# Kernel tuning notes

Hardware: AMD Instinct MI355X
Metric: run time of the kernel (lower is better)

Reference implementation:

```python
import jax, jax.numpy as jnp
import numpy as np
from jax import lax

B, L, D, H = 2, 2048, 2048, 16
DH = D // H            # 128 head dim
D_REL = 64             # relevance projection dim (class const)
K = max(1, int(0.25 * L))  # top-K_FRAC tokens per query
NEG_INF = float('-inf')


def setup_inputs() -> dict:
    key = jax.random.key(0)
    ks = jax.random.split(key, 8)
    s = D ** (-0.5)
    return {
        'hidden_states': jax.random.normal(ks[0], (B, L, D), jnp.float32),
        'relevance':     jax.random.normal(ks[1], (B, L, D), jnp.float32),
        # torch nn.Linear weights are [out_features, in_features]
        'W_q_rel': jax.random.normal(ks[2], (D_REL, D), jnp.float32) * s,
        'W_k_rel': jax.random.normal(ks[3], (D_REL, D), jnp.float32) * s,
        'W_q': jax.random.normal(ks[4], (D, D), jnp.float32) * s,
        'W_k': jax.random.normal(ks[5], (D, D), jnp.float32) * s,
        'W_v': jax.random.normal(ks[6], (D, D), jnp.float32) * s,
        'W_o': jax.random.normal(ks[7], (D, D), jnp.float32) * s,
    }


def _rel_scores(relevance, W_q_rel, W_k_rel):
    # low-rank relevance logits, causally masked: [B, L, L]
    q = relevance @ W_q_rel.T   # [B, L, d_rel]
    k = relevance @ W_k_rel.T   # [B, L, d_rel]
    scores = jnp.einsum('bqd,bkd->bqk', q, k) * (D_REL ** -0.5)
    future = jnp.triu(jnp.ones((L, L), dtype=bool), k=1)
    return jnp.where(future[None], NEG_INF, scores)


def _sparse_mask(rel_scores):
    # additive mask [B, 1, L, L]: top-k per query row -> 0.0, else -inf; diag 0.0
    _, topk_idx = lax.top_k(rel_scores, K)            # [B, L, K]
    b = jnp.arange(B)[:, None, None]
    q = jnp.arange(L)[None, :, None]
    mask = jnp.full((B, L, L), NEG_INF, dtype=rel_scores.dtype)
    mask = mask.at[b, q, topk_idx].set(0.0)
    diag = jnp.arange(L)
    mask = mask.at[:, diag, diag].set(0.0)
    return mask[:, None]  # [B, 1, L, L]


def _attention(hidden_states, W_q, W_k, W_v, W_o, add_mask):
    # standard multi-head attention with additive mask (the wrapped frozen attn)
    q = (hidden_states @ W_q.T).reshape(B, L, H, DH)
    k = (hidden_states @ W_k.T).reshape(B, L, H, DH)
    v = (hidden_states @ W_v.T).reshape(B, L, H, DH)
    scores = jnp.einsum('bqhd,bkhd->bhqk', q, k) * (DH ** -0.5)
    scores = scores + add_mask                      # [B, H, L, L]
    p = jax.nn.softmax(scores, axis=-1)
    ctx = jnp.einsum('bhqk,bkhd->bqhd', p, v).reshape(B, L, D)
    return ctx @ W_o.T


def reference(hidden_states, relevance, W_q_rel, W_k_rel, W_q, W_k, W_v, W_o):
    # Phase 1 path (step >= SPARSE_FROM), no external attention_mask:
    # combined = causal(-inf upper-tri) + sparse top-k mask.
    rel = _rel_scores(relevance, W_q_rel, W_k_rel)
    sparse = _sparse_mask(rel)                      # [B, 1, L, L]
    future = jnp.triu(jnp.ones((L, L), dtype=bool), k=1)
    causal = jnp.where(future, NEG_INF, 0.0).astype(hidden_states.dtype)
    combined = causal[None, None] + sparse          # [B, 1, L, L]
    return _attention(hidden_states, W_q, W_k, W_v, W_o, combined)
```

## Files before the change

### kernel.cpp

```cpp
#include <hip/hip_runtime.h>
#include <math.h>
#include <stdint.h>

#define Bb 2
#define Lq 2048
#define Dm 2048
#define Hh 16
#define DH 128
#define DREL 64
#define KTOP 512

#define NEG_INF (-__builtin_huge_valf())

typedef __attribute__((ext_vector_type(8))) short bf16x8;
typedef __attribute__((ext_vector_type(4))) float f32x4;

static __device__ __forceinline__ unsigned short f2bf(float f) {
  unsigned int u = __float_as_uint(f);
  u += 0x7fffu + ((u >> 16) & 1u);
  return (unsigned short)(u >> 16);
}

static __device__ __forceinline__ void gload16(const void* g, void* lds) {
  __builtin_amdgcn_global_load_lds(
      (const __attribute__((address_space(1))) uint32_t*)(uintptr_t)g,
      (__attribute__((address_space(3))) uint32_t*)(uint32_t)(uintptr_t)lds,
      16, 0, 0);
}

__global__ __launch_bounds__(256) void conv_bf16(const float* __restrict__ in,
                                                 unsigned short* __restrict__ out,
                                                 int n8, float scale) {
  const int i = blockIdx.x * 256 + threadIdx.x;
  if (i >= n8) return;
  const float4 f0 = ((const float4*)in)[2 * i];
  const float4 f1 = ((const float4*)in)[2 * i + 1];
  bf16x8 o;
  o[0] = (short)f2bf(f0.x * scale); o[1] = (short)f2bf(f0.y * scale);
  o[2] = (short)f2bf(f0.z * scale); o[3] = (short)f2bf(f0.w * scale);
  o[4] = (short)f2bf(f1.x * scale); o[5] = (short)f2bf(f1.y * scale);
  o[6] = (short)f2bf(f1.z * scale); o[7] = (short)f2bf(f1.w * scale);
  *(bf16x8*)(out + 8 * (size_t)i) = o;
}

__global__ __launch_bounds__(256) void conv_bf16_w4(const float* __restrict__ w0,
                                                    const float* __restrict__ w1,
                                                    const float* __restrict__ w2,
                                                    const float* __restrict__ w3,
                                                    unsigned short* __restrict__ out,
                                                    float s0) {
  const int sel = blockIdx.y;
  const float* in = (sel == 0) ? w0 : (sel == 1) ? w1 : (sel == 2) ? w2 : w3;
  const float scale = (sel == 0) ? s0 : 1.0f;
  const int i = blockIdx.x * 256 + threadIdx.x;
  const float4 f0 = ((const float4*)in)[2 * i];
  const float4 f1 = ((const float4*)in)[2 * i + 1];
  bf16x8 o;
  o[0] = (short)f2bf(f0.x * scale); o[1] = (short)f2bf(f0.y * scale);
  o[2] = (short)f2bf(f0.z * scale); o[3] = (short)f2bf(f0.w * scale);
  o[4] = (short)f2bf(f1.x * scale); o[5] = (short)f2bf(f1.y * scale);
  o[6] = (short)f2bf(f1.z * scale); o[7] = (short)f2bf(f1.w * scale);
  *(bf16x8*)(out + (size_t)sel * Dm * Dm + 8 * (size_t)i) = o;
}

template <int MF, bool BF16OUT>
__global__ __launch_bounds__(512, 4) void gemmP(const unsigned short* __restrict__ A,
                                                const unsigned short* __restrict__ W,
                                                void* __restrict__ Cv,
                                                int M, int N, int Kd) {
  constexpr int BM = MF * 32;
  __shared__ unsigned short As[2][BM][32];
  __shared__ unsigned short Bs[2][256][32];

  const int tid = threadIdx.x;
  const int lane = tid & 63;
  const int w = tid >> 6;
  const int l15 = lane & 15;
  const int quad = lane >> 4;
  const int wm = w >> 2;
  const int wn = w & 3;

  const int gy = M / BM;
  const int nwg = gy * (N >> 8);
  const int cpx = nwg >> 3;
  const int bid = (int)blockIdx.x;
  const int lin = (bid & 7) * cpx + (bid >> 3);
  const int by = lin % gy, bx = lin / gy;
  const int m0 = by * BM, n0 = bx * 256;

  const int srow = tid >> 2;
  const int sslot = (tid & 3) ^ ((tid >> 3) & 3);
  const unsigned short* aB = A + (size_t)(m0 + srow) * Kd + sslot * 8;
  const unsigned short* bB = W + (size_t)(n0 + srow) * Kd + sslot * 8;
  const size_t hstep = (size_t)128 * Kd;

  f32x4 acc[MF][4];
#pragma unroll
  for (int i = 0; i < MF; ++i)
#pragma unroll
    for (int j = 0; j < 4; ++j) acc[i][j] = (f32x4){0.f, 0.f, 0.f, 0.f};

  bf16x8 af[MF], bfr[2];
  const int rswz = (quad ^ ((l15 >> 1) & 3)) * 8;

#define ST(BUF, T)                                                          \
  do {                                                                      \
    const size_t ko = (size_t)(T) * 32;                                     \
    gload16(aB + ko, &As[BUF][w * 16][0]);                                  \
    if constexpr (MF == 8) gload16(aB + hstep + ko, &As[BUF][(MF == 8 ? 128 : 0) + w * 16][0]); \
    gload16(bB + ko, &Bs[BUF][w * 16][0]);                                  \
    gload16(bB + hstep + ko, &Bs[BUF][128 + w * 16][0]);                    \
  } while (0)

#define LD_A(BUF)                                                           \
  _Pragma("unroll") for (int mi = 0; mi < MF; ++mi)                         \
      af[mi] = *(const bf16x8*)&As[BUF][wm * (BM / 2) + mi * 16 + l15][rswz];

#define LD_B(BUF, NP)                                                       \
  _Pragma("unroll") for (int ni = 0; ni < 2; ++ni)                          \
      bfr[ni] = *(const bf16x8*)&Bs[BUF][wn * 64 + ((NP) * 2 + ni) * 16 + l15][rswz];

#define MFMA_NP(NP)                                                         \
  do {                                                                      \
    __builtin_amdgcn_s_setprio(1);                                          \
    _Pragma("unroll") for (int mi = 0; mi < MF; ++mi)                       \
        _Pragma("unroll") for (int ni = 0; ni < 2; ++ni)                    \
            acc[mi][(NP) * 2 + ni] = __builtin_amdgcn_mfma_f32_16x16x32_bf16( \
                af[mi], bfr[ni], acc[mi][(NP) * 2 + ni], 0, 0, 0);          \
    __builtin_amdgcn_s_setprio(0);                                          \
  } while (0)

  ST(0, 0);

  const int nt = Kd >> 5;
  int buf = 0;
  for (int t = 0; t < nt; ++t) {
    if (t + 1 < nt) {
      ST(buf ^ 1, t + 1);
      if constexpr (MF == 8)
        asm volatile("s_waitcnt vmcnt(4)\ns_barrier" ::: "memory");
      else
        asm volatile("s_waitcnt vmcnt(3)\ns_barrier" ::: "memory");
    } else {
      asm volatile("s_waitcnt vmcnt(0)\ns_barrier" ::: "memory");
    }
    LD_A(buf);
    LD_B(buf, 0);
    MFMA_NP(0);
    LD_B(buf, 1);
    MFMA_NP(1);
    asm volatile("s_barrier" ::: "memory");
    buf ^= 1;
  }
#undef ST
#undef LD_A
#undef LD_B
#undef MFMA_NP

#pragma unroll
  for (int im = 0; im < MF; ++im) {
#pragma unroll
    for (int in = 0; in < 4; ++in) {
      const int col = n0 + wn * 64 + in * 16 + l15;
#pragma unroll
      for (int r = 0; r < 4; ++r) {
        const int row = m0 + wm * (BM / 2) + im * 16 + quad * 4 + r;
        if (BF16OUT)
          ((unsigned short*)Cv)[(size_t)row * N + col] = f2bf(acc[im][in][r]);
        else
          ((float*)Cv)[(size_t)row * N + col] = acc[im][in][r];
      }
    }
  }
}

#define RKS 8
__global__ __launch_bounds__(256) void relproj2(const float* __restrict__ A,
                                                const float* __restrict__ Wqr,
                                                const float* __restrict__ Wkr,
                                                float* __restrict__ partq,
                                                float* __restrict__ partk, int M) {
  const float* W = blockIdx.z ? Wkr : Wqr;
  float* part = blockIdx.z ? partk : partq;
  __shared__ float As[16][128];
  __shared__ float Bs[16][64];
  const int ks = blockIdx.x;
  const int m0 = blockIdx.y * 128;
  const int tid = threadIdx.x;
  const int tx = tid & 15;
  const int ty = tid >> 4;
  const int lr = tid >> 1, lk = (tid & 1) * 8;
  const int wr = tid >> 2, wk = (tid & 3) * 4;

  float acc[8][4];
#pragma unroll
  for (int i = 0; i < 8; ++i)
#pragma unroll
    for (int j = 0; j < 4; ++j) acc[i][j] = 0.f;

  const int k00 = ks * (Dm / RKS);
  for (int k0 = k00; k0 < k00 + Dm / RKS; k0 += 16) {
    {
      const float* ap = A + (size_t)(m0 + lr) * Dm + k0 + lk;
      float4 a0 = *(const float4*)(ap);
      float4 a1 = *(const float4*)(ap + 4);
      As[lk + 0][lr] = a0.x; As[lk + 1][lr] = a0.y;
      As[lk + 2][lr] = a0.z; As[lk + 3][lr] = a0.w;
      As[lk + 4][lr] = a1.x; As[lk + 5][lr] = a1.y;
      As[lk + 6][lr] = a1.z; As[lk + 7][lr] = a1.w;
    }
    {
      const float* bp = W + (size_t)wr * Dm + k0 + wk;
      float4 b0 = *(const float4*)(bp);
      Bs[wk + 0][wr] = b0.x; Bs[wk + 1][wr] = b0.y;
      Bs[wk + 2][wr] = b0.z; Bs[wk + 3][wr] = b0.w;
    }
    __syncthreads();
#pragma unroll
    for (int kk = 0; kk < 16; ++kk) {
      float af[8], bf[4];
#pragma unroll
      for (int i = 0; i < 8; ++i) af[i] = As[kk][ty * 8 + i];
#pragma unroll
      for (int j = 0; j < 4; ++j) bf[j] = Bs[kk][tx * 4 + j];
#pragma unroll
      for (int i = 0; i < 8; ++i)
#pragma unroll
        for (int j = 0; j < 4; ++j) acc[i][j] += af[i] * bf[j];
    }
    __syncthreads();
  }

#pragma unroll
  for (int i = 0; i < 8; ++i) {
    float* pp = part + ((size_t)ks * M + m0 + ty * 8 + i) * DREL + tx * 4;
    *(float4*)pp = make_float4(acc[i][0], acc[i][1], acc[i][2], acc[i][3]);
  }
}

__global__ __launch_bounds__(256) void relreduce(const float* __restrict__ pq,
                                                 const float* __restrict__ pk,
                                                 float* __restrict__ qrel,
                                                 float* __restrict__ krel, int n4) {
  const int i = blockIdx.x * 256 + threadIdx.x;
  if (i >= n4) return;
  float4 sq = make_float4(0, 0, 0, 0), sk = sq;
  for (int s = 0; s < RKS; ++s) {
    float4 a = ((const float4*)pq)[(size_t)s * n4 + i];
    float4 b = ((const float4*)pk)[(size_t)s * n4 + i];
    sq.x += a.x; sq.y += a.y; sq.z += a.z; sq.w += a.w;
    sk.x += b.x; sk.y += b.y; sk.z += b.z; sk.w += b.w;
  }
  ((float4*)qrel)[i] = sq;
  ((float4*)krel)[i] = sk;
}

__global__ __launch_bounds__(256) void relscore(const float* __restrict__ qrel,
                                                const float* __restrict__ krel,
                                                float* __restrict__ S) {
  const int jt = blockIdx.x, qt = blockIdx.y, b = blockIdx.z;
  if (jt > qt) return;
  __shared__ float As[16][128];
  __shared__ float Bs[16][128];
  const int tid = threadIdx.x;
  const int q0 = qt * 128, j0 = jt * 128;
  const int tx = tid & 15, ty = tid >> 4;
  const int lr = tid >> 1, lk = (tid & 1) * 8;
  const float* Ab = qrel + (size_t)b * Lq * DREL;
  const float* Kb = krel + (size_t)b * Lq * DREL;

  float acc[8][8];
#pragma unroll
  for (int i = 0; i < 8; ++i)
#pragma unroll
    for (int j = 0; j < 8; ++j) acc[i][j] = 0.f;

  for (int k0 = 0; k0 < DREL; k0 += 16) {
    {
      const float* ap = Ab + (size_t)(q0 + lr) * DREL + k0 + lk;
      float4 a0 = *(const float4*)(ap);
      float4 a1 = *(const float4*)(ap + 4);
      As[lk + 0][lr] = a0.x; As[lk + 1][lr] = a0.y;
      As[lk + 2][lr] = a0.z; As[lk + 3][lr] = a0.w;
      As[lk + 4][lr] = a1.x; As[lk + 5][lr] = a1.y;
      As[lk + 6][lr] = a1.z; As[lk + 7][lr] = a1.w;
    }
    {
      const float* bp = Kb + (size_t)(j0 + lr) * DREL + k0 + lk;
      float4 b0 = *(const float4*)(bp);
      float4 b1 = *(const float4*)(bp + 4);
      Bs[lk + 0][lr] = b0.x; Bs[lk + 1][lr] = b0.y;
      Bs[lk + 2][lr] = b0.z; Bs[lk + 3][lr] = b0.w;
      Bs[lk + 4][lr] = b1.x; Bs[lk + 5][lr] = b1.y;
      Bs[lk + 6][lr] = b1.z; Bs[lk + 7][lr] = b1.w;
    }
    __syncthreads();
#pragma unroll
    for (int kk = 0; kk < 16; ++kk) {
      float af[8], bf[8];
#pragma unroll
      for (int i = 0; i < 8; ++i) af[i] = As[kk][ty * 8 + i];
#pragma unroll
      for (int j = 0; j < 8; ++j) bf[j] = Bs[kk][tx * 8 + j];
#pragma unroll
      for (int i = 0; i < 8; ++i)
#pragma unroll
        for (int j = 0; j < 8; ++j) acc[i][j] += af[i] * bf[j];
    }
    __syncthreads();
  }

  const float sc = 0.125f;
#pragma unroll
  for (int i = 0; i < 8; ++i) {
    float* cp = S + ((size_t)b * Lq + q0 + ty * 8 + i) * Lq + j0 + tx * 8;
    ((float4*)cp)[0] = make_float4(acc[i][0] * sc, acc[i][1] * sc, acc[i][2] * sc, acc[i][3] * sc);
    ((float4*)cp)[1] = make_float4(acc[i][4] * sc, acc[i][5] * sc, acc[i][6] * sc, acc[i][7] * sc);
  }
}

__global__ __launch_bounds__(256) void relselect(const float* __restrict__ S,
                                                 uint32_t* __restrict__ mask) {
  const int w = threadIdx.x >> 6;
  const int lane = threadIdx.x & 63;
  const int ridx = blockIdx.x * 4 + w;
  const int qi = ridx & (Lq - 1);
  const int n = qi + 1;
  const float* srow = S + (size_t)ridx * Lq;

  uint32_t keys[32];
#pragma unroll
  for (int t = 0; t < 32; ++t) {
    const int j = t * 64 + lane;
    const uint32_t u = __float_as_uint(srow[j]);
    const uint32_t k = (u & 0x80000000u) ? ~u : (u | 0x80000000u);
    keys[t] = (j < n) ? k : 0u;
  }

  uint32_t kth = 0u;
  if (n > KTOP) {
    uint32_t pref = 0u;
    int rem = KTOP;
    for (int bit = 31; bit >= 0; --bit) {
      const uint32_t cand = pref | (1u << bit);
      const uint32_t lim = 1u << bit;
      int c = 0;
#pragma unroll
      for (int t = 0; t < 32; ++t) c += ((keys[t] ^ cand) < lim) ? 1 : 0;
      c += __shfl_xor(c, 1);
      c += __shfl_xor(c, 2);
      c += __shfl_xor(c, 4);
      c += __shfl_xor(c, 8);
      c += __shfl_xor(c, 16);
      c += __shfl_xor(c, 32);
      if (c >= rem) pref = cand;
      else rem -= c;
    }
    kth = pref;
  }

  uint32_t* mrow = mask + (size_t)ridx * (Lq / 32);
#pragma unroll
  for (int t = 0; t < 32; ++t) {
    const int j = t * 64 + lane;
    const bool ok = (j < n) && (keys[t] >= kth || j == qi);
    const unsigned long long bal = __ballot(ok);
    if (lane == 0) {
      mrow[2 * t] = (uint32_t)bal;
      mrow[2 * t + 1] = (uint32_t)(bal >> 32);
    }
  }
}

#define ATQ 128
#define TK 64
__global__ __launch_bounds__(512, 4) void attn_flash3(const unsigned short* __restrict__ qkv,
                                                      const uint32_t* __restrict__ mask,
                                                      unsigned short* __restrict__ ctx) {
  __shared__ unsigned short Ks[2][TK][136];
  __shared__ unsigned short Vt[2][2][64][72];
  __shared__ uint32_t mw[2][ATQ][2];

  const int qt = (blockIdx.z == 0) ? ((Lq / ATQ) - 1 - (int)blockIdx.x) : (int)blockIdx.x;
  const int h = blockIdx.y;
  const int b = blockIdx.z;
  const int tid = threadIdx.x;
  const int w = tid >> 6;
  const int lane = tid & 63;
  const int l15 = lane & 15;
  const int quad = lane >> 4;
  const int q0 = qt * ATQ;
  const int STR = 3 * Dm;

  const unsigned short* kbp = qkv + 2048;
  const unsigned short* vbp = qkv + 4096;

  const int myq = q0 + w * 16 + l15;
  const unsigned short* qrow = qkv + (size_t)(b * Lq + myq) * STR + h * DH;
  bf16x8 bq[4];
#pragma unroll
  for (int kk = 0; kk < 4; ++kk) bq[kk] = *(const bf16x8*)(qrow + kk * 32 + quad * 8);

  f32x4 O[8];
#pragma unroll
  for (int f = 0; f < 8; ++f) O[f] = (f32x4){0.f, 0.f, 0.f, 0.f};
  float l_lane = 0.f;

  const int nt = (q0 + ATQ) / TK;

  const int skey = (tid & 255) >> 2;
  const int scg  = tid & 3;
  const int mq   = (tid & 255) >> 1;
  const int msel = tid & 1;
  const int tv = tid - 256;
  const int vkp = tv & 31;
  const int vdg = (tv >> 5) & 7;
  const int vhalf = vkp >> 4;
  const int vkp16 = vkp & 15;
  const int dwc = ((vkp16 >> 1) & 3) * 4 + (vkp16 >> 3) * 2 + (vkp16 & 1);

  const uint32_t* mrow_base = mask + (size_t)(b * Lq + q0 + mq) * (Lq / 32) + msel;
  const unsigned short* krow_base = kbp + (size_t)(b * Lq + skey) * STR + h * DH + scg * 32;
  const unsigned short* vrow_base = vbp + (size_t)(b * Lq + 2 * vkp) * STR + h * DH + vdg * 16;

  bf16x8 r0, r1, r2, r3;
  uint32_t mreg = 0;

#define LOADREGS(KT)                                                       \
  do {                                                                     \
    const int kbase_ = (KT) * TK;                                          \
    if (tid < 256) {                                                       \
      const unsigned short* kr = krow_base + (size_t)kbase_ * STR;         \
      r0 = *(const bf16x8*)(kr);                                           \
      r1 = *(const bf16x8*)(kr + 8);                                       \
      r2 = *(const bf16x8*)(kr + 16);                                      \
      r3 = *(const bf16x8*)(kr + 24);                                      \
      mreg = mrow_base[(KT) * 2];                                          \
    } else {                                                               \
      const unsigned short* vr = vrow_base + (size_t)kbase_ * STR;         \
      r0 = *(const bf16x8*)(vr);                                           \
      r1 = *(const bf16x8*)(vr + 8);                                       \
      r2 = *(const bf16x8*)(vr + STR);                                     \
      r3 = *(const bf16x8*)(vr + STR + 8);                                 \
    }                                                                      \
  } while (0)

#define WRITELDS(BUF)                                                      \
  do {                                                                     \
    if (tid < 256) {                                                       \
      *(bf16x8*)&Ks[BUF][skey][scg * 32 + 0]  = r0;                        \
      *(bf16x8*)&Ks[BUF][skey][scg * 32 + 8]  = r1;                        \
      *(bf16x8*)&Ks[BUF][skey][scg * 32 + 16] = r2;                        \
      *(bf16x8*)&Ks[BUF][skey][scg * 32 + 24] = r3;                        \
      mw[BUF][mq][msel] = mreg;                                            \
    } else {                                                               \
      _Pragma("unroll") for (int i = 0; i < 8; ++i) {                      \
        const int d = vdg * 16 + i;                                        \
        const uint32_t pk = (uint32_t)(unsigned short)r0[i] |              \
                            ((uint32_t)(unsigned short)r2[i] << 16);       \
        ((uint32_t*)&Vt[BUF][vhalf][d >> 1][0])[(d & 1) * 16 + dwc] = pk;  \
      }                                                                    \
      _Pragma("unroll") for (int i = 0; i < 8; ++i) {                      \
        const int d = vdg * 16 + 8 + i;                                    \
        const uint32_t pk = (uint32_t)(unsigned short)r1[i] |              \
                            ((uint32_t)(unsigned short)r3[i] << 16);       \
        ((uint32_t*)&Vt[BUF][vhalf][d >> 1][0])[(d & 1) * 16 + dwc] = pk;  \
      }                                                                    \
    }                                                                      \
  } while (0)

  LOADREGS(0);
  WRITELDS(0);
  __syncthreads();

  int buf = 0;
  for (int kt = 0; kt < nt; ++kt) {
    const bool more = (kt + 1 < nt);
    if (more) LOADREGS(kt + 1);

    __builtin_amdgcn_s_setprio(1);
#pragma unroll
    for (int hh = 0; hh < 2; ++hh) {
      f32x4 acc0 = (f32x4){0.f, 0.f, 0.f, 0.f};
      f32x4 acc1 = acc0;
#pragma unroll
      for (int kk = 0; kk < 4; ++kk) {
        bf16x8 a0 = *(const bf16x8*)&Ks[buf][hh * 32 + l15][kk * 32 + quad * 8];
        bf16x8 a1 = *(const bf16x8*)&Ks[buf][hh * 32 + 16 + l15][kk * 32 + quad * 8];
        acc0 = __builtin_amdgcn_mfma_f32_16x16x32_bf16(a0, bq[kk], acc0, 0, 0, 0);
        acc1 = __builtin_amdgcn_mfma_f32_16x16x32_bf16(a1, bq[kk], acc1, 0, 0, 0);
      }

      const uint32_t mword = mw[buf][w * 16 + l15][hh];
      bf16x8 bp;
      float ps = 0.f;
#pragma unroll
      for (int r = 0; r < 4; ++r) {
        const float p0 = ((mword >> (quad * 4 + r)) & 1u) ? __builtin_amdgcn_exp2f(acc0[r]) : 0.f;
        const float p1 = ((mword >> (16 + quad * 4 + r)) & 1u) ? __builtin_amdgcn_exp2f(acc1[r]) : 0.f;
        ps += p0 + p1;
        bp[r] = (short)f2bf(p0);
        bp[4 + r] = (short)f2bf(p1);
      }
      l_lane += ps;

#pragma unroll
      for (int f = 0; f < 8; ++f) {
        const int d = f * 16 + l15;
        bf16x8 av = *(const bf16x8*)&Vt[buf][hh][d >> 1][(d & 1) * 32 + quad * 8];
        O[f] = __builtin_amdgcn_mfma_f32_16x16x32_bf16(av, bp, O[f], 0, 0, 0);
      }
    }
    __builtin_amdgcn_s_setprio(0);

    if (more) WRITELDS(buf ^ 1);
    __syncthreads();
    buf ^= 1;
  }
#undef LOADREGS
#undef WRITELDS

  l_lane += __shfl_xor(l_lane, 16);
  l_lane += __shfl_xor(l_lane, 32);
  const float rl = 1.0f / l_lane;

  unsigned short* orow = ctx + ((size_t)(b * Lq + q0 + w * 16 + l15)) * Dm + h * DH;
#pragma unroll
  for (int f = 0; f < 8; ++f) {
    ushort4 o4;
    o4.x = f2bf(O[f][0] * rl);
    o4.y = f2bf(O[f][1] * rl);
    o4.z = f2bf(O[f][2] * rl);
    o4.w = f2bf(O[f][3] * rl);
    *(ushort4*)(orow + f * 16 + quad * 4) = o4;
  }
}

extern "C" void kernel_launch(void* const* d_in, const int* in_sizes, int n_in,
                              void* d_out, int out_size, void* d_ws, size_t ws_size,
                              hipStream_t stream) {
  const float* hs  = (const float*)d_in[0];
  const float* rel = (const float*)d_in[1];
  const float* Wqr = (const float*)d_in[2];
  const float* Wkr = (const float*)d_in[3];
  const float* Wq  = (const float*)d_in[4];
  const float* Wk  = (const float*)d_in[5];
  const float* Wv  = (const float*)d_in[6];
  const float* Wo  = (const float*)d_in[7];
  float* out = (float*)d_out;

  const int M = Bb * Lq;
  const int ND = Dm * Dm;
  char* ws = (char*)d_ws;
  size_t off = 0;
  float* qrel = (float*)(ws + off); off += (size_t)M * DREL * 4;
  float* krel = (float*)(ws + off); off += (size_t)M * DREL * 4;
  uint32_t* maskb = (uint32_t*)(ws + off); off += (size_t)M * (Lq / 32) * 4;
  float* partq = (float*)(ws + off); off += (size_t)RKS * M * DREL * 4;
  float* partk = (float*)(ws + off); off += (size_t)RKS * M * DREL * 4;
  float* Sbuf = (float*)(ws + off);
  unsigned short* hsb  = (unsigned short*)(ws + off); off += (size_t)M * Dm * 2;
  unsigned short* qkvb = (unsigned short*)(ws + off); off += (size_t)M * 3 * Dm * 2;
  unsigned short* ctxb = (unsigned short*)(ws + off); off += (size_t)M * Dm * 2;
  unsigned short* Wqkvo = (unsigned short*)(ws + off); off += (size_t)4 * ND * 2;

  const dim3 blk(256);
  const int hsN8 = M * Dm / 8;
  const float QSCALE = 0.08838834764831845f * 1.4426950408889634f;

  relproj2<<<dim3(RKS, M / 128, 2), blk, 0, stream>>>(rel, Wqr, Wkr, partq, partk, M);
  relreduce<<<(M * DREL / 4 + 255) / 256, blk, 0, stream>>>(partq, partk, qrel, krel, M * DREL / 4);
  relscore<<<dim3(Lq / 128, Lq / 128, Bb), blk, 0, stream>>>(qrel, krel, Sbuf);
  relselect<<<M / 4, blk, 0, stream>>>(Sbuf, maskb);

  conv_bf16<<<(hsN8 + 255) / 256, blk, 0, stream>>>(hs, hsb, hsN8, 1.0f);
  conv_bf16_w4<<<dim3(ND / 8 / 256, 4), blk, 0, stream>>>(Wq, Wk, Wv, Wo, Wqkvo, QSCALE);

  gemmP<4, true><<<dim3((M / 128) * (3 * Dm / 256)), dim3(512), 0, stream>>>(
      hsb, Wqkvo, qkvb, M, 3 * Dm, Dm);

  attn_flash3<<<dim3(Lq / ATQ, Hh, Bb), dim3(512), 0, stream>>>(qkvb, maskb, ctxb);

  gemmP<4, false><<<dim3((M / 128) * (Dm / 256)), dim3(512), 0, stream>>>(
      ctxb, Wqkvo + (size_t)3 * ND, out, M, Dm, Dm);
}
```

Baseline: 475.4 us.

## Replace 128x256 GEMM with 128x128 tile, 256 threads, triple-buffered LDS pipeline

Replaces the 512-thread 128x256 GEMM with a 256-thread 128x128 tile kernel that keeps three LDS stages and prefetches two K-steps ahead. The goal is to hide global-load latency better and to launch more workgroups for the QKV and output projections. Each wave still computes a 64x64 sub-tile. In exchange, A and B panels are re-read more often because the tile is smaller, and the extra LDS per block may limit occupancy.

```diff
diff --git a/kernel.cpp b/kernel.cpp
--- a/kernel.cpp
+++ b/kernel.cpp
@@ -63,58 +63,57 @@
   *(bf16x8*)(out + (size_t)sel * Dm * Dm + 8 * (size_t)i) = o;
 }
 
-template <int MF, bool BF16OUT>
-__global__ __launch_bounds__(512, 4) void gemmP(const unsigned short* __restrict__ A,
+template <bool BF16OUT>
+__global__ __launch_bounds__(256, 3) void gemmT(const unsigned short* __restrict__ A,
                                                 const unsigned short* __restrict__ W,
                                                 void* __restrict__ Cv,
                                                 int M, int N, int Kd) {
-  constexpr int BM = MF * 32;
-  __shared__ unsigned short As[2][BM][32];
-  __shared__ unsigned short Bs[2][256][32];
+  __shared__ unsigned short As[3][128][32];
+  __shared__ unsigned short Bs[3][128][32];
 
   const int tid = threadIdx.x;
   const int lane = tid & 63;
   const int w = tid >> 6;
   const int l15 = lane & 15;
   const int quad = lane >> 4;
-  const int wm = w >> 2;
-  const int wn = w & 3;
-
-  const int gy = M / BM;
-  const int nwg = gy * (N >> 8);
+  const int wm = w >> 1;
+  const int wn = w & 1;
+
+  const int gy = M >> 7;
+  const int nwg = gy * (N >> 7);
   const int cpx = nwg >> 3;
   const int bid = (int)blockIdx.x;
   const int lin = (bid & 7) * cpx + (bid >> 3);
   const int by = lin % gy, bx = lin / gy;
-  const int m0 = by * BM, n0 = bx * 256;
+  const int m0 = by * 128, n0 = bx * 128;
 
   const int srow = tid >> 2;
   const int sslot = (tid & 3) ^ ((tid >> 3) & 3);
   const unsigned short* aB = A + (size_t)(m0 + srow) * Kd + sslot * 8;
   const unsigned short* bB = W + (size_t)(n0 + srow) * Kd + sslot * 8;
-  const size_t hstep = (size_t)128 * Kd;
-
-  f32x4 acc[MF][4];
-#pragma unroll
-  for (int i = 0; i < MF; ++i)
+  const size_t hstep = (size_t)64 * Kd;
+
+  f32x4 acc[4][4];
+#pragma unroll
+  for (int i = 0; i < 4; ++i)
 #pragma unroll
     for (int j = 0; j < 4; ++j) acc[i][j] = (f32x4){0.f, 0.f, 0.f, 0.f};
 
-  bf16x8 af[MF], bfr[2];
+  bf16x8 af[4], bfr[2];
   const int rswz = (quad ^ ((l15 >> 1) & 3)) * 8;
 
 #define ST(BUF, T)                                                          \
   do {                                                                      \
     const size_t ko = (size_t)(T) * 32;                                     \
     gload16(aB + ko, &As[BUF][w * 16][0]);                                  \
-    if constexpr (MF == 8) gload16(aB + hstep + ko, &As[BUF][(MF == 8 ? 128 : 0) + w * 16][0]); \
+    gload16(aB + hstep + ko, &As[BUF][64 + w * 16][0]);                     \
     gload16(bB + ko, &Bs[BUF][w * 16][0]);                                  \
-    gload16(bB + hstep + ko, &Bs[BUF][128 + w * 16][0]);                    \
+    gload16(bB + hstep + ko, &Bs[BUF][64 + w * 16][0]);                     \
   } while (0)
 
 #define LD_A(BUF)                                                           \
-  _Pragma("unroll") for (int mi = 0; mi < MF; ++mi)                         \
-      af[mi] = *(const bf16x8*)&As[BUF][wm * (BM / 2) + mi * 16 + l15][rswz];
+  _Pragma("unroll") for (int mi = 0; mi < 4; ++mi)                          \
+      af[mi] = *(const bf16x8*)&As[BUF][wm * 64 + mi * 16 + l15][rswz];
 
 #define LD_B(BUF, NP)                                                       \
   _Pragma("unroll") for (int ni = 0; ni < 2; ++ni)                          \
@@ -123,7 +122,7 @@
 #define MFMA_NP(NP)                                                         \
   do {                                                                      \
     __builtin_amdgcn_s_setprio(1);                                          \
-    _Pragma("unroll") for (int mi = 0; mi < MF; ++mi)                       \
+    _Pragma("unroll") for (int mi = 0; mi < 4; ++mi)                        \
         _Pragma("unroll") for (int ni = 0; ni < 2; ++ni)                    \
             acc[mi][(NP) * 2 + ni] = __builtin_amdgcn_mfma_f32_16x16x32_bf16( \
                 af[mi], bfr[ni], acc[mi][(NP) * 2 + ni], 0, 0, 0);          \
@@ -131,26 +130,27 @@
   } while (0)
 
   ST(0, 0);
+  ST(1, 1);
 
   const int nt = Kd >> 5;
-  int buf = 0;
+  int cb = 0;
   for (int t = 0; t < nt; ++t) {
-    if (t + 1 < nt) {
-      ST(buf ^ 1, t + 1);
-      if constexpr (MF == 8)
-        asm volatile("s_waitcnt vmcnt(4)\ns_barrier" ::: "memory");
-      else
-        asm volatile("s_waitcnt vmcnt(3)\ns_barrier" ::: "memory");
+    if (t + 2 < nt) {
+      const int sb = (cb >= 1) ? (cb - 1) : 2;
+      ST(sb, t + 2);
+      asm volatile("s_waitcnt vmcnt(8)\ns_barrier" ::: "memory");
+    } else if (t + 1 < nt) {
+      asm volatile("s_waitcnt vmcnt(4)\ns_barrier" ::: "memory");
     } else {
       asm volatile("s_waitcnt vmcnt(0)\ns_barrier" ::: "memory");
     }
-    LD_A(buf);
-    LD_B(buf, 0);
+    LD_A(cb);
+    LD_B(cb, 0);
     MFMA_NP(0);
-    LD_B(buf, 1);
+    LD_B(cb, 1);
     MFMA_NP(1);
     asm volatile("s_barrier" ::: "memory");
-    buf ^= 1;
+    cb = (cb + 1 == 3) ? 0 : cb + 1;
   }
 #undef ST
 #undef LD_A
@@ -158,13 +158,13 @@
 #undef MFMA_NP
 
 #pragma unroll
-  for (int im = 0; im < MF; ++im) {
+  for (int im = 0; im < 4; ++im) {
 #pragma unroll
     for (int in = 0; in < 4; ++in) {
       const int col = n0 + wn * 64 + in * 16 + l15;
 #pragma unroll
       for (int r = 0; r < 4; ++r) {
-        const int row = m0 + wm * (BM / 2) + im * 16 + quad * 4 + r;
+        const int row = m0 + wm * 64 + im * 16 + quad * 4 + r;
         if (BF16OUT)
           ((unsigned short*)Cv)[(size_t)row * N + col] = f2bf(acc[im][in][r]);
         else
@@ -576,11 +576,11 @@
   conv_bf16<<<(hsN8 + 255) / 256, blk, 0, stream>>>(hs, hsb, hsN8, 1.0f);
   conv_bf16_w4<<<dim3(ND / 8 / 256, 4), blk, 0, stream>>>(Wq, Wk, Wv, Wo, Wqkvo, QSCALE);
 
-  gemmP<4, true><<<dim3((M / 128) * (3 * Dm / 256)), dim3(512), 0, stream>>>(
+  gemmT<true><<<dim3((M / 128) * (3 * Dm / 128)), blk, 0, stream>>>(
       hsb, Wqkvo, qkvb, M, 3 * Dm, Dm);
 
   attn_flash3<<<dim3(Lq / ATQ, Hh, Bb), dim3(512), 0, stream>>>(qkvb, maskb, ctxb);
 
-  gemmP<4, false><<<dim3((M / 128) * (Dm / 256)), dim3(512), 0, stream>>>(
+  gemmT<false><<<dim3((M / 128) * (Dm / 128)), blk, 0, stream>>>(
       ctxb, Wqkvo + (size_t)3 * ND, out, M, Dm, Dm);
 }
```

Result: slower. 485.5 us (+2.1%).
